# Kernel optimization log

Hardware: AMD Instinct MI355X
Metric: run time of the kernel (lower is better)

## Reference

```python
import jax, jax.numpy as jnp
import numpy as np

BN_EPS = 1e-5
ELU_ALPHA = 512.0  # bug-faithful: nn.ELU(in_channels) sets alpha=in_channels


def conv3x3(x, w):
    # NCHW input, OIHW kernel, stride 1, padding 1 (SAME for k=3)
    return jax.lax.conv_general_dilated(
        x, w, window_strides=(1, 1), padding=((1, 1), (1, 1)),
        dimension_numbers=('NCHW', 'OIHW', 'NCHW'))


def conv1x1(x, w, b):
    # 1x1 conv as a channel contraction
    return jnp.einsum('oc,bchw->bohw', w[:, :, 0, 0], x) + b[None, :, None, None]


def batchnorm(x, g, b, m, v):
    scale = g / jnp.sqrt(v + BN_EPS)
    return (x - m[None, :, None, None]) * scale[None, :, None, None] + b[None, :, None, None]


def cc_module(x, wq, bq, wk, bk, wv, bv, gamma):
    B, C, H, W = x.shape
    q = conv1x1(x, wq, bq)   # [B, C/8, H, W]
    k = conv1x1(x, wk, bk)   # [B, C/8, H, W]
    v = conv1x1(x, wv, bv)   # [B, C,   H, W]
    # column (H-axis) attention scores with -inf on the self-diagonal
    eH = jnp.einsum('bchw,bcgw->bhwg', q, k)              # [B,H,W,H]
    diag = jnp.eye(H, dtype=bool)[None, :, None, :]       # mask h == g
    eH = jnp.where(diag, -jnp.inf, eH)
    # row (W-axis) attention scores
    eW = jnp.einsum('bchw,bchv->bhwv', q, k)              # [B,H,W,W]
    att = jax.nn.softmax(jnp.concatenate([eH, eW], axis=-1), axis=-1)  # [B,H,W,H+W]
    aH, aW = att[..., :H], att[..., H:]
    oH = jnp.einsum('bcgw,bhwg->bchw', v, aH)
    oW = jnp.einsum('bchv,bhwv->bchw', v, aW)
    return gamma[0] * (oH + oW) + x


def setup_inputs() -> dict:
    key = jax.random.key(0)
    ks = jax.random.split(key, 20)
    B, Cin, H, W = 8, 512, 64, 64
    Ci = Cin // 4            # 128
    Cq = Ci // 8             # 16
    n = lambda k, s, sc: jax.random.normal(k, s, dtype=jnp.float32) * sc
    inp = {
        'x': n(ks[0], (B, Cin, H, W), 1.0),
        'conva_w': n(ks[1], (Ci, Cin, 3, 3), 0.02),
        'bn1_g': jax.random.uniform(ks[2], (Ci,)) + 0.5,
        'bn1_b': n(ks[3], (Ci,), 0.1),
        'bn1_m': n(ks[4], (Ci,), 0.1),
        'bn1_v': jax.random.uniform(ks[5], (Ci,)) + 0.5,
        'wq': n(ks[6], (Cq, Ci, 1, 1), 0.05),
        'bq': n(ks[7], (Cq,), 0.02),
        'wk': n(ks[8], (Cq, Ci, 1, 1), 0.05),
        'bk': n(ks[9], (Cq,), 0.02),
        'wv': n(ks[10], (Ci, Ci, 1, 1), 0.05),
        'bv': n(ks[11], (Ci,), 0.02),
        'cc_gamma': jnp.full((1,), 0.5, dtype=jnp.float32),
        'convb_w': n(ks[12], (Ci, Ci, 3, 3), 0.05),
        'bn2_g': jax.random.uniform(ks[13], (Ci,)) + 0.5,
        'bn2_b': n(ks[14], (Ci,), 0.1),
        'bn2_m': n(ks[15], (Ci,), 0.1),
        'bn2_v': jax.random.uniform(ks[16], (Ci,)) + 0.5,
        'bott_w': n(ks[17], (Cin, Cin + Ci, 3, 3), 0.02),
        'recurrence': 2,
    }
    return inp


def reference(x, conva_w, bn1_g, bn1_b, bn1_m, bn1_v,
              wq, bq, wk, bk, wv, bv, cc_gamma,
              convb_w, bn2_g, bn2_b, bn2_m, bn2_v,
              bott_w, recurrence):
    out = batchnorm(conv3x3(x, conva_w), bn1_g, bn1_b, bn1_m, bn1_v)
    for _ in range(int(recurrence)):
        out = cc_module(out, wq, bq, wk, bk, wv, bv, cc_gamma)
    out = batchnorm(conv3x3(out, convb_w), bn2_g, bn2_b, bn2_m, bn2_v)
    out = conv3x3(jnp.concatenate([x, out], axis=1), bott_w)
    # ELU with alpha = in_channels (faithful to nn.ELU(in_channels))
    return jnp.where(out > 0, out, ELU_ALPHA * jnp.expm1(out))
```

## Files before the change

### kernel.cpp

```cpp
#include <hip/hip_runtime.h>
#include <math.h>


typedef __attribute__((ext_vector_type(8)))  short short8;
typedef __attribute__((ext_vector_type(4)))  float f32x4;
typedef __attribute__((ext_vector_type(16))) float f32x16;

__device__ __forceinline__ unsigned short f2bf(float x) {
    unsigned u = __float_as_uint(x);
    unsigned r = u + 0x7FFFu + ((u >> 16) & 1u);
    return (unsigned short)(r >> 16);
}
__device__ __forceinline__ float bf2f(unsigned short h) {
    return __uint_as_float(((unsigned)h) << 16);
}
__device__ __forceinline__ void split2(float a, float b, unsigned& hi, unsigned& lo) {
    unsigned h;
    asm("v_cvt_pk_bf16_f32 %0, %1, %2" : "=v"(h) : "v"(a), "v"(b));
    float ra = a - __uint_as_float(h << 16);
    float rb = b - __uint_as_float(h & 0xffff0000u);
    unsigned l;
    asm("v_cvt_pk_bf16_f32 %0, %1, %2" : "=v"(l) : "v"(ra), "v"(rb));
    hi = h; lo = l;
}
__device__ __forceinline__ void gll16(const unsigned short* g, unsigned short* l) {
    __builtin_amdgcn_global_load_lds(
        (const __attribute__((address_space(1))) unsigned int*)g,
        (__attribute__((address_space(3))) unsigned int*)l, 16, 0, 0);
}

__global__ __launch_bounds__(256) void prep_bn_kernel(
        const float* g1, const float* b1, const float* m1, const float* v1,
        const float* g2, const float* b2, const float* m2, const float* v2,
        float* s1o, float* h1o, float* s2o, float* h2o) {
    int t = threadIdx.x;
    if (t < 128) {
        float s = g1[t] * __frsqrt_rn(v1[t] + 1e-5f);
        s1o[t] = s; h1o[t] = b1[t] - m1[t] * s;
    } else {
        int c = t - 128;
        float s = g2[c] * __frsqrt_rn(v2[c] + 1e-5f);
        s2o[c] = s; h2o[c] = b2[c] - m2[c] * s;
    }
}

__global__ __launch_bounds__(256) void prep_w2(
        const float* __restrict__ w, unsigned short* __restrict__ Wp, int CIN, int COUT) {
    int idx = blockIdx.x * 256 + threadIdx.x;
    if (idx >= COUT * CIN) return;
    int cout = idx / CIN, ci = idx - cout * CIN;
    int ck = ci >> 5, cl = ci & 31;
    #pragma unroll
    for (int tap = 0; tap < 9; ++tap) {
        float v = w[(size_t)idx * 9 + tap];
        unsigned short h = f2bf(v);
        unsigned short l = f2bf(v - bf2f(h));
        size_t rb = (((size_t)ck * 9 + tap) * 2 * COUT + cout) * 32;
        Wp[rb + cl] = h;
        Wp[rb + (size_t)COUT * 32 + cl] = l;
    }
}

__global__ __launch_bounds__(256) void prep_qkv_kernel(
        const float* __restrict__ wq, const float* __restrict__ wk,
        const float* __restrict__ wv,
        float* __restrict__ wqk_t, float* __restrict__ wv_t) {
    int e = blockIdx.x * 256 + threadIdx.x;
    if (e < 4096) {
        int ci = e >> 5, co = e & 31;
        wqk_t[e] = (co < 16) ? wq[co * 128 + ci] : wk[(co - 16) * 128 + ci];
    } else if (e < 4096 + 16384) {
        int e2 = e - 4096;
        int ci = e2 >> 7, co = e2 & 127;
        wv_t[e2] = wv[co * 128 + ci];
    }
}

__global__ __launch_bounds__(256) void transpose_split_kernel(
        const float* __restrict__ in, unsigned short* __restrict__ out, int NCH) {
    __shared__ float T[32][260];
    const int t = threadIdx.x;
    const int h0 = blockIdx.x * 4, b = blockIdx.y, ck = blockIdx.z;
    const float* base = in + (size_t)(b * NCH + ck) * 32 * 4096;
    const int ci = t >> 3, w0 = (t & 7) * 8;
    #pragma unroll
    for (int hh = 0; hh < 4; ++hh) {
        float4 u0 = *(const float4*)&base[(size_t)ci * 4096 + (h0 + hh) * 64 + w0];
        float4 u1 = *(const float4*)&base[(size_t)ci * 4096 + (h0 + hh) * 64 + w0 + 4];
        T[ci][hh * 65 + w0 + 0] = u0.x; T[ci][hh * 65 + w0 + 1] = u0.y;
        T[ci][hh * 65 + w0 + 2] = u0.z; T[ci][hh * 65 + w0 + 3] = u0.w;
        T[ci][hh * 65 + w0 + 4] = u1.x; T[ci][hh * 65 + w0 + 5] = u1.y;
        T[ci][hh * 65 + w0 + 6] = u1.z; T[ci][hh * 65 + w0 + 7] = u1.w;
    }
    __syncthreads();
    const int w = t & 63, hh2 = t >> 6;
    const int h = h0 + hh2;
    const size_t PL = (size_t)64 * 68 * 40;
    unsigned short* po = out + ((size_t)(b * NCH + ck) * 2) * PL;
    unsigned hi[16], lo[16];
    #pragma unroll
    for (int p = 0; p < 16; ++p) {
        float a = T[2 * p][hh2 * 65 + w];
        float c = T[2 * p + 1][hh2 * 65 + w];
        split2(a, c, hi[p], lo[p]);
    }
    uint4 zz = {0u, 0u, 0u, 0u};
    #pragma unroll
    for (int half = 0; half < 2; ++half) {
        bool ok = half ? (w >= 31) : (w <= 32);
        int slot = half ? (w - 31) : (w + 1);
        if (ok) {
            unsigned short* ph = po + ((size_t)h * 68 + half * 34 + slot) * 40;
            unsigned short* pl = ph + PL;
            #pragma unroll
            for (int q = 0; q < 4; ++q) {
                uint4 hv = {hi[q * 4], hi[q * 4 + 1], hi[q * 4 + 2], hi[q * 4 + 3]};
                uint4 lv = {lo[q * 4], lo[q * 4 + 1], lo[q * 4 + 2], lo[q * 4 + 3]};
                *(uint4*)(ph + q * 8) = hv;
                *(uint4*)(pl + q * 8) = lv;
            }
            *(uint4*)(ph + 32) = zz;
            *(uint4*)(pl + 32) = zz;
        }
    }
    if (w == 0 || w == 63) {
        int half = (w == 63);
        int slot = half ? 33 : 0;
        unsigned short* ph = po + ((size_t)h * 68 + half * 34 + slot) * 40;
        #pragma unroll
        for (int q = 0; q < 5; ++q) {
            *(uint4*)(ph + q * 8) = zz;
            *(uint4*)(ph + PL + q * 8) = zz;
        }
    }
}

template<int NCHUNK, int COUT, int EPI, int C1CH>
__global__ __launch_bounds__(128, 2) void conv3x3_g(
        const unsigned short* __restrict__ xt1, const unsigned short* __restrict__ xt2,
        const unsigned short* __restrict__ Wp,
        const float* __restrict__ bns, const float* __restrict__ bnb,
        float* __restrict__ out) {
    __shared__ __align__(16) unsigned short XS[2][6][34][40];
    const int t = threadIdx.x;
    const int lane = t & 63, ch = t >> 6;
    const int lw = lane & 31, kg = lane >> 5;
    const int h0 = blockIdx.x * 4;
    const int b  = blockIdx.y;
    const int cz = blockIdx.z >> 1, wz = blockIdx.z & 1;
    const int cb0 = cz * 128;
    const size_t XPLANE = (size_t)64 * 68 * 40;
    constexpr int HLSTR = 6 * 34 * 40;

    const f32x16 fz = {0.f,0.f,0.f,0.f,0.f,0.f,0.f,0.f,0.f,0.f,0.f,0.f,0.f,0.f,0.f,0.f};
    f32x16 acc[2][4];
    #pragma unroll
    for (int mt = 0; mt < 2; ++mt)
        #pragma unroll
        for (int r = 0; r < 4; ++r) acc[mt][r] = fz;

    #pragma unroll 1
    for (int chunk = 0; chunk < NCHUNK; ++chunk) {
        const unsigned short* xb = (chunk < C1CH)
            ? xt1 + ((size_t)(b * C1CH + chunk) * 2) * XPLANE
            : xt2 + ((size_t)(b * (NCHUNK - C1CH) + (chunk - C1CH)) * 2) * XPLANE;
        #pragma unroll
        for (int j = 0; j < 6; ++j) {
            const int grow = h0 - 1 + j;
            unsigned short* ld = &XS[ch][j][0][0];
            if (grow >= 0 && grow < 64) {
                const unsigned short* g = xb + (size_t)ch * XPLANE + ((size_t)grow * 68 + wz * 34) * 40;
                gll16(g + (size_t)lane * 8, ld + (size_t)lane * 8);
                gll16(g + (size_t)(64 + lane) * 8, ld + (size_t)(64 + lane) * 8);
                if (lane < 42)
                    gll16(g + (size_t)(128 + lane) * 8, ld + (size_t)(128 + lane) * 8);
            } else {
                short8 z = {};
                *(short8*)(ld + (size_t)lane * 8) = z;
                *(short8*)(ld + (size_t)(64 + lane) * 8) = z;
                if (lane < 42) *(short8*)(ld + (size_t)(128 + lane) * 8) = z;
            }
        }
        __syncthreads();

        const unsigned short* wbase = Wp + (size_t)chunk * (9 * 2 * (size_t)COUT * 32);
        const int crow = cb0 + ch * 64 + lw;
        short8 wc[8], wn[8];
        {
            const unsigned short* ph = wbase + ((size_t)0 * COUT + crow) * 32 + kg * 8;
            const unsigned short* pl = ph + (size_t)COUT * 32;
            wc[0] = *(const short8*)(ph);             wc[1] = *(const short8*)(ph + 32 * 32);
            wc[2] = *(const short8*)(pl);             wc[3] = *(const short8*)(pl + 32 * 32);
            wc[4] = *(const short8*)(ph + 16);        wc[5] = *(const short8*)(ph + 32 * 32 + 16);
            wc[6] = *(const short8*)(pl + 16);        wc[7] = *(const short8*)(pl + 32 * 32 + 16);
        }
        #pragma unroll 1
        for (int tap = 0; tap < 9; ++tap) {
            {
                const int tn = (tap < 8) ? tap + 1 : 0;
                const unsigned short* ph = wbase + ((size_t)(tn * 2) * COUT + crow) * 32 + kg * 8;
                const unsigned short* pl = ph + (size_t)COUT * 32;
                wn[0] = *(const short8*)(ph);         wn[1] = *(const short8*)(ph + 32 * 32);
                wn[2] = *(const short8*)(pl);         wn[3] = *(const short8*)(pl + 32 * 32);
                wn[4] = *(const short8*)(ph + 16);    wn[5] = *(const short8*)(ph + 32 * 32 + 16);
                wn[6] = *(const short8*)(pl + 16);    wn[7] = *(const short8*)(pl + 32 * 32 + 16);
            }
            const int kh = (tap < 3) ? 0 : ((tap < 6) ? 1 : 2);
            const int kw = tap - kh * 3;
            #pragma unroll
            for (int ks = 0; ks < 2; ++ks) {
                const short8 ah0 = wc[ks * 4 + 0], ah1 = wc[ks * 4 + 1];
                const short8 al0 = wc[ks * 4 + 2], al1 = wc[ks * 4 + 3];
                const int ko = ks * 16 + kg * 8;
                #pragma unroll
                for (int r = 0; r < 4; ++r) {
                    const unsigned short* xp = &XS[0][r + kh][lw + kw][ko];
                    short8 bh = *(const short8*)xp;
                    short8 bl = *(const short8*)(xp + HLSTR);
                    acc[0][r] = __builtin_amdgcn_mfma_f32_32x32x16_bf16(ah0, bh, acc[0][r], 0, 0, 0);
                    acc[1][r] = __builtin_amdgcn_mfma_f32_32x32x16_bf16(ah1, bh, acc[1][r], 0, 0, 0);
                    acc[0][r] = __builtin_amdgcn_mfma_f32_32x32x16_bf16(ah0, bl, acc[0][r], 0, 0, 0);
                    acc[1][r] = __builtin_amdgcn_mfma_f32_32x32x16_bf16(ah1, bl, acc[1][r], 0, 0, 0);
                    acc[0][r] = __builtin_amdgcn_mfma_f32_32x32x16_bf16(al0, bh, acc[0][r], 0, 0, 0);
                    acc[1][r] = __builtin_amdgcn_mfma_f32_32x32x16_bf16(al1, bh, acc[1][r], 0, 0, 0);
                }
            }
            #pragma unroll
            for (int i = 0; i < 8; ++i) wc[i] = wn[i];
        }
        __syncthreads();
    }
    #pragma unroll
    for (int mt = 0; mt < 2; ++mt) {
        #pragma unroll
        for (int r = 0; r < 4; ++r) {
            const int orow = h0 + r;
            #pragma unroll
            for (int reg = 0; reg < 16; ++reg) {
                const int m = (reg & 3) + 8 * (reg >> 2) + 4 * kg;
                const int cout = cb0 + ch * 64 + mt * 32 + m;
                float val = acc[mt][r][reg];
                if (EPI == 0) val = val * bns[cout] + bnb[cout];
                else          val = (val > 0.f) ? val : 512.0f * expm1f(val);
                out[((size_t)(b * COUT + cout) * 64 + orow) * 64 + wz * 32 + lw] = val;
            }
        }
    }
}

__global__ __launch_bounds__(256) void qk_kernel(
        const float* __restrict__ X, const float* __restrict__ wqk_t,
        const float* __restrict__ bq, const float* __restrict__ bk,
        float* __restrict__ q, float* __restrict__ k) {
    __shared__ float xls[128][64];
    __shared__ float wls[128][32];
    const int t = threadIdx.x;
    const int h = blockIdx.x, b = blockIdx.y;
    const float* xb = X + (size_t)b * 128 * 4096 + (size_t)h * 64;
    #pragma unroll
    for (int i = 0; i < 32; ++i) {
        int e = t + i * 256;
        xls[e >> 6][e & 63] = xb[(size_t)(e >> 6) * 4096 + (e & 63)];
    }
    #pragma unroll
    for (int i = 0; i < 16; ++i) {
        int e = t + i * 256;
        wls[e >> 5][e & 31] = wqk_t[e];
    }
    __syncthreads();
    const int w = t & 63, g = t >> 6;
    const int co0 = g * 8;
    float acc[8];
    #pragma unroll
    for (int c = 0; c < 8; ++c) acc[c] = 0.f;
    #pragma unroll 8
    for (int ci = 0; ci < 128; ++ci) {
        float xv = xls[ci][w];
        float4 wa = *(const float4*)&wls[ci][co0];
        float4 wb = *(const float4*)&wls[ci][co0 + 4];
        const float* pa = (const float*)&wa;
        const float* pb = (const float*)&wb;
        #pragma unroll
        for (int c = 0; c < 4; ++c) { acc[c] += pa[c] * xv; acc[4 + c] += pb[c] * xv; }
    }
    #pragma unroll
    for (int c = 0; c < 8; ++c) {
        int co = co0 + c;
        if (co < 16) q[((size_t)(b * 16 + co) * 64 + h) * 64 + w]      = acc[c] + bq[co];
        else         k[((size_t)(b * 16 + co - 16) * 64 + h) * 64 + w] = acc[c] + bk[co - 16];
    }
}

__global__ __launch_bounds__(256) void v_kernel(
        const float* __restrict__ X, const float* __restrict__ wv_t,
        const float* __restrict__ bv, float* __restrict__ v) {
    __shared__ float xls[16][64];
    __shared__ float wls[16][128];
    const int t = threadIdx.x;
    const int n0 = blockIdx.x * 64, b = blockIdx.y;
    const int wt = t & 15, ct = t >> 4;
    const float* xb = X + (size_t)b * 128 * 4096;
    float acc[8][4] = {};
    for (int ci0 = 0; ci0 < 128; ci0 += 16) {
        #pragma unroll
        for (int i = 0; i < 4; ++i) {
            int e = t + i * 256;
            xls[e >> 6][e & 63] = xb[(size_t)(ci0 + (e >> 6)) * 4096 + n0 + (e & 63)];
        }
        #pragma unroll
        for (int i = 0; i < 8; ++i) {
            int e = t + i * 256;
            wls[e >> 7][e & 127] = wv_t[(size_t)(ci0 + (e >> 7)) * 128 + (e & 127)];
        }
        __syncthreads();
        #pragma unroll 4
        for (int ci = 0; ci < 16; ++ci) {
            float4 xv = *(const float4*)&xls[ci][wt * 4];
            float4 wa = *(const float4*)&wls[ci][ct * 8];
            float4 wb = *(const float4*)&wls[ci][ct * 8 + 4];
            const float* px = (const float*)&xv;
            const float* pa = (const float*)&wa;
            const float* pb = (const float*)&wb;
            #pragma unroll
            for (int j = 0; j < 4; ++j)
                #pragma unroll
                for (int c = 0; c < 4; ++c) {
                    acc[c][j]     += pa[c] * px[j];
                    acc[4 + c][j] += pb[c] * px[j];
                }
        }
        __syncthreads();
    }
    #pragma unroll
    for (int c = 0; c < 8; ++c) {
        int co = ct * 8 + c;
        float bb = bv[co];
        float4 r = {acc[c][0] + bb, acc[c][1] + bb, acc[c][2] + bb, acc[c][3] + bb};
        *(float4*)&v[(size_t)(b * 128 + co) * 4096 + n0 + wt * 4] = r;
    }
}

__global__ __launch_bounds__(256) void eh_kernel(
        const float* __restrict__ q, const float* __restrict__ k,
        float* __restrict__ att) {
    __shared__ float qs[16][64];
    __shared__ float ks[16][64];
    const int t = threadIdx.x;
    const int w = blockIdx.x, b = blockIdx.y;
    #pragma unroll
    for (int i = 0; i < 4; ++i) {
        int e = t + i * 256;
        int c = e >> 6, h = e & 63;
        size_t idx = ((size_t)(b * 16 + c) * 64 + h) * 64 + w;
        qs[c][h] = q[idx];
        ks[c][h] = k[idx];
    }
    __syncthreads();
    const int g0 = (t & 15) * 4, h0 = (t >> 4) * 4;
    float acc[4][4] = {};
    #pragma unroll
    for (int c = 0; c < 16; ++c) {
        float4 qv = *(const float4*)&qs[c][h0];
        float4 kv = *(const float4*)&ks[c][g0];
        const float* pq = (const float*)&qv;
        const float* pk = (const float*)&kv;
        #pragma unroll
        for (int i = 0; i < 4; ++i)
            #pragma unroll
            for (int j = 0; j < 4; ++j) acc[i][j] += pq[i] * pk[j];
    }
    #pragma unroll
    for (int i = 0; i < 4; ++i) {
        int h = h0 + i;
        int dj = h - g0;
        if (dj >= 0 && dj < 4) acc[i][dj] = -1e30f;
        float4 r = {acc[i][0], acc[i][1], acc[i][2], acc[i][3]};
        *(float4*)&att[((size_t)(b * 64 + h) * 64 + w) * 128 + g0] = r;
    }
}

__global__ __launch_bounds__(256) void ew_softmax_kernel(
        const float* __restrict__ q, const float* __restrict__ k,
        float* __restrict__ att) {
    __shared__ float qs[16][64];
    __shared__ float ks[16][64];
    __shared__ float ehs[64][65];
    __shared__ float ews[64][65];
    __shared__ float sinv[64];
    const int t = threadIdx.x;
    const int h = blockIdx.x, b = blockIdx.y;
    const float* qb2 = q + (size_t)b * 65536 + (size_t)h * 64;
    const float* kb2 = k + (size_t)b * 65536 + (size_t)h * 64;
    #pragma unroll
    for (int i = 0; i < 4; ++i) {
        int e = t + i * 256;
        int c = e >> 6, wl = e & 63;
        qs[c][wl] = qb2[(size_t)c * 4096 + wl];
        ks[c][wl] = kb2[(size_t)c * 4096 + wl];
    }
    float* abase = att + (size_t)(b * 64 + h) * 64 * 128;
    #pragma unroll
    for (int i = 0; i < 16; ++i) {
        int e = t + i * 256;
        ehs[e >> 6][e & 63] = abase[(size_t)(e >> 6) * 128 + (e & 63)];
    }
    __syncthreads();
    const int tt0 = (t & 15) * 4, w0 = (t >> 4) * 4;
    float acc[4][4] = {};
    #pragma unroll
    for (int c = 0; c < 16; ++c) {
        float4 qv = *(const float4*)&qs[c][w0];
        float4 kv = *(const float4*)&ks[c][tt0];
        const float* pq = (const float*)&qv;
        const float* pk = (const float*)&kv;
        #pragma unroll
        for (int i = 0; i < 4; ++i)
            #pragma unroll
            for (int j = 0; j < 4; ++j) acc[i][j] += pq[i] * pk[j];
    }
    #pragma unroll
    for (int i = 0; i < 4; ++i)
        #pragma unroll
        for (int j = 0; j < 4; ++j) ews[w0 + i][tt0 + j] = acc[i][j];
    __syncthreads();
    const int r = t >> 2, qd = t & 3;
    float* src = (qd < 2) ? &ehs[r][qd * 32] : &ews[r][(qd - 2) * 32];
    float m = -3.0e38f;
    #pragma unroll
    for (int kk = 0; kk < 32; ++kk) m = fmaxf(m, src[kk]);
    m = fmaxf(m, __shfl_xor(m, 1));
    m = fmaxf(m, __shfl_xor(m, 2));
    float s = 0.f;
    #pragma unroll
    for (int kk = 0; kk < 32; ++kk) {
        float e = expf(src[kk] - m);
        src[kk] = e;
        s += e;
    }
    s += __shfl_xor(s, 1);
    s += __shfl_xor(s, 2);
    if (qd == 0) sinv[r] = 1.0f / s;
    __syncthreads();
    #pragma unroll
    for (int i = 0; i < 32; ++i) {
        int e = t + i * 256;
        int row = e >> 7, col = e & 127;
        float vsm = (col < 64) ? ehs[row][col] : ews[row][col - 64];
        abase[(size_t)row * 128 + col] = vsm * sinv[row];
    }
}

__global__ __launch_bounds__(256) void oh_kernel(
        const float* __restrict__ v, const float* __restrict__ att,
        float* __restrict__ ohb) {
    __shared__ float vs2[64][128];
    __shared__ float ah2[64][65];
    const int t = threadIdx.x;
    const int w = blockIdx.x, b = blockIdx.y;
    const float* vbp = v + (size_t)b * 524288 + w;
    #pragma unroll
    for (int i = 0; i < 32; ++i) {
        int e = t + i * 256;
        vs2[e >> 7][e & 127] = vbp[((size_t)(e & 127) * 64 + (e >> 7)) * 64];
    }
    const float* abp = att + ((size_t)b * 4096 + w) * 128;
    #pragma unroll
    for (int i = 0; i < 16; ++i) {
        int e = t + i * 256;
        ah2[e >> 6][e & 63] = abp[(size_t)(e >> 6) * 8192 + (e & 63)];
    }
    __syncthreads();
    const int h0 = (t & 15) * 4, c0 = (t >> 4) * 8;
    float acc[8][4] = {};
    for (int g = 0; g < 64; ++g) {
        float4 va  = *(const float4*)&vs2[g][c0];
        float4 vb4 = *(const float4*)&vs2[g][c0 + 4];
        const float* pa = (const float*)&va;
        const float* pb = (const float*)&vb4;
        float aj[4];
        #pragma unroll
        for (int j = 0; j < 4; ++j) aj[j] = ah2[h0 + j][g];
        #pragma unroll
        for (int j = 0; j < 4; ++j)
            #pragma unroll
            for (int i2 = 0; i2 < 4; ++i2) {
                acc[i2][j]     += pa[i2] * aj[j];
                acc[4 + i2][j] += pb[i2] * aj[j];
            }
    }
    #pragma unroll
    for (int i2 = 0; i2 < 8; ++i2)
        #pragma unroll
        for (int j = 0; j < 4; ++j)
            ohb[((size_t)(b * 128 + c0 + i2) * 64 + (h0 + j)) * 64 + w] = acc[i2][j];
}

__global__ __launch_bounds__(256) void ow_final_kernel(
        const float* __restrict__ v, const float* __restrict__ att,
        const float* __restrict__ ohb, const float* __restrict__ gamma,
        const float* __restrict__ Xin, float* __restrict__ Xout) {
    __shared__ float vs2[64][129];
    __shared__ float aws[64][65];
    const int t = threadIdx.x;
    const int h = blockIdx.x, b = blockIdx.y;
    const float* vbp = v + (size_t)b * 524288 + (size_t)h * 64;
    #pragma unroll
    for (int i = 0; i < 32; ++i) {
        int e = t + i * 256;
        vs2[e & 63][e >> 6] = vbp[(size_t)(e >> 6) * 4096 + (e & 63)];
    }
    const float* abp = att + ((size_t)(b * 64 + h) * 64) * 128 + 64;
    #pragma unroll
    for (int i = 0; i < 16; ++i) {
        int e = t + i * 256;
        aws[e >> 6][e & 63] = abp[(size_t)(e >> 6) * 128 + (e & 63)];
    }
    __syncthreads();
    const int w0 = (t & 15) * 4, c0 = (t >> 4) * 8;
    float acc[8][4] = {};
    for (int tt = 0; tt < 64; ++tt) {
        float vv[8];
        #pragma unroll
        for (int i2 = 0; i2 < 8; ++i2) vv[i2] = vs2[tt][c0 + i2];
        float aw[4];
        #pragma unroll
        for (int j = 0; j < 4; ++j) aw[j] = aws[w0 + j][tt];
        #pragma unroll
        for (int i2 = 0; i2 < 8; ++i2)
            #pragma unroll
            for (int j = 0; j < 4; ++j) acc[i2][j] += vv[i2] * aw[j];
    }
    const float gm = gamma[0];
    #pragma unroll
    for (int i2 = 0; i2 < 8; ++i2) {
        size_t base = ((size_t)(b * 128 + c0 + i2) * 64 + h) * 64 + w0;
        float4 oh4 = *(const float4*)&ohb[base];
        float4 xr  = *(const float4*)&Xin[base];
        const float* po = (const float*)&oh4;
        const float* px = (const float*)&xr;
        float4 r;
        float* pr = (float*)&r;
        #pragma unroll
        for (int j = 0; j < 4; ++j) pr[j] = gm * (acc[i2][j] + po[j]) + px[j];
        *(float4*)&Xout[base] = r;
    }
}

extern "C" void kernel_launch(void* const* d_in, const int* in_sizes, int n_in,
                              void* d_out, int out_size, void* d_ws, size_t ws_size,
                              hipStream_t stream) {
    const float* x       = (const float*)d_in[0];
    const float* conva_w = (const float*)d_in[1];
    const float* bn1_g   = (const float*)d_in[2];
    const float* bn1_b   = (const float*)d_in[3];
    const float* bn1_m   = (const float*)d_in[4];
    const float* bn1_v   = (const float*)d_in[5];
    const float* wq      = (const float*)d_in[6];
    const float* bq      = (const float*)d_in[7];
    const float* wk      = (const float*)d_in[8];
    const float* bk      = (const float*)d_in[9];
    const float* wv      = (const float*)d_in[10];
    const float* bv      = (const float*)d_in[11];
    const float* gamma   = (const float*)d_in[12];
    const float* convb_w = (const float*)d_in[13];
    const float* bn2_g   = (const float*)d_in[14];
    const float* bn2_b   = (const float*)d_in[15];
    const float* bn2_m   = (const float*)d_in[16];
    const float* bn2_v   = (const float*)d_in[17];
    const float* bott_w  = (const float*)d_in[18];

    float* ws   = (float*)d_ws;
    float* A    = ws;
    float* Bb   = A    + 4194304;
    float* vbuf = Bb   + 4194304;
    float* attb = vbuf + 4194304;
    float* ohb  = attb + 4194304;
    float* qb   = ohb  + 4194304;
    float* kb   = qb   + 524288;
    unsigned short* XT_x = (unsigned short*)(kb + 524288);
    float* after_xt = kb + 524288 + 22282240;
    unsigned short* Wp_a = (unsigned short*)after_xt;
    unsigned short* Wp_b = Wp_a + 1179648;
    unsigned short* Wp_c = Wp_b + 294912;
    float* wqk_t = (float*)(Wp_c + 5898240);
    float* wv_t  = wqk_t + 4096;
    float* bnsA  = wv_t + 16384;
    float* bnbA  = bnsA + 128;
    float* bnsB  = bnbA + 128;
    float* bnbB  = bnsB + 128;
    unsigned short* XT_cc = (unsigned short*)vbuf;
    unsigned short* XT_b  = XT_cc + 11141120;

    prep_bn_kernel<<<1, 256, 0, stream>>>(bn1_g, bn1_b, bn1_m, bn1_v,
                                          bn2_g, bn2_b, bn2_m, bn2_v,
                                          bnsA, bnbA, bnsB, bnbB);
    prep_w2<<<256, 256, 0, stream>>>(conva_w, Wp_a, 512, 128);
    prep_w2<<<64, 256, 0, stream>>>(convb_w, Wp_b, 128, 128);
    prep_w2<<<1280, 256, 0, stream>>>(bott_w, Wp_c, 640, 512);
    prep_qkv_kernel<<<80, 256, 0, stream>>>(wq, wk, wv, wqk_t, wv_t);

    transpose_split_kernel<<<dim3(16, 8, 16), 256, 0, stream>>>(x, XT_x, 16);

    conv3x3_g<16, 128, 0, 16><<<dim3(16, 8, 2), 128, 0, stream>>>(
        XT_x, nullptr, Wp_a, bnsA, bnbA, A);

    float* Xi = A;
    float* Xo = Bb;
    for (int it = 0; it < 2; ++it) {
        qk_kernel<<<dim3(64, 8), 256, 0, stream>>>(Xi, wqk_t, bq, bk, qb, kb);
        v_kernel<<<dim3(64, 8), 256, 0, stream>>>(Xi, wv_t, bv, vbuf);
        eh_kernel<<<dim3(64, 8), 256, 0, stream>>>(qb, kb, attb);
        ew_softmax_kernel<<<dim3(64, 8), 256, 0, stream>>>(qb, kb, attb);
        oh_kernel<<<dim3(64, 8), 256, 0, stream>>>(vbuf, attb, ohb);
        ow_final_kernel<<<dim3(64, 8), 256, 0, stream>>>(vbuf, attb, ohb, gamma, Xi, Xo);
        float* tmp = Xi; Xi = Xo; Xo = tmp;
    }

    transpose_split_kernel<<<dim3(16, 8, 4), 256, 0, stream>>>(Xi, XT_cc, 4);
    conv3x3_g<4, 128, 0, 4><<<dim3(16, 8, 2), 128, 0, stream>>>(
        XT_cc, nullptr, Wp_b, bnsB, bnbB, Bb);

    transpose_split_kernel<<<dim3(16, 8, 4), 256, 0, stream>>>(Bb, XT_b, 4);
    conv3x3_g<20, 512, 1, 16><<<dim3(16, 8, 8), 128, 0, stream>>>(
        XT_x, XT_b, Wp_c, nullptr, nullptr, (float*)d_out);
}
```

Measured before the change: 1.227 ms.

## Halve conv3x3 row tile, raise occupancy, make weight prefetch optional per launch

Each conv3x3 block now computes 2 output rows instead of 4, which halves the accumulator registers and shared-memory tile and doubles the grid. Launch bounds are raised to target 3–4 blocks per CU. A PF template flag lets the bottleneck conv skip the register double-buffered weight prefetch and load weights directly per k-step, saving registers. The MFMA issue order is regrouped so independent accumulators interleave. The trade-off is that each block reuses its weights and halo rows less, so more input rows are reloaded overall.

```diff
diff --git a/kernel.cpp b/kernel.cpp
--- a/kernel.cpp
+++ b/kernel.cpp
@@ -135,29 +135,29 @@
     }
 }
 
-template<int NCHUNK, int COUT, int EPI, int C1CH>
-__global__ __launch_bounds__(128, 2) void conv3x3_g(
+template<int NCHUNK, int COUT, int EPI, int C1CH, int PF>
+__global__ __launch_bounds__(128, PF ? 3 : 4) void conv3x3_g(
         const unsigned short* __restrict__ xt1, const unsigned short* __restrict__ xt2,
         const unsigned short* __restrict__ Wp,
         const float* __restrict__ bns, const float* __restrict__ bnb,
         float* __restrict__ out) {
-    __shared__ __align__(16) unsigned short XS[2][6][34][40];
+    __shared__ __align__(16) unsigned short XS[2][4][34][40];
     const int t = threadIdx.x;
     const int lane = t & 63, ch = t >> 6;
     const int lw = lane & 31, kg = lane >> 5;
-    const int h0 = blockIdx.x * 4;
+    const int h0 = blockIdx.x * 2;
     const int b  = blockIdx.y;
     const int cz = blockIdx.z >> 1, wz = blockIdx.z & 1;
     const int cb0 = cz * 128;
     const size_t XPLANE = (size_t)64 * 68 * 40;
-    constexpr int HLSTR = 6 * 34 * 40;
+    constexpr int HLSTR = 4 * 34 * 40;
 
     const f32x16 fz = {0.f,0.f,0.f,0.f,0.f,0.f,0.f,0.f,0.f,0.f,0.f,0.f,0.f,0.f,0.f,0.f};
-    f32x16 acc[2][4];
+    f32x16 acc[2][2];
     #pragma unroll
     for (int mt = 0; mt < 2; ++mt)
         #pragma unroll
-        for (int r = 0; r < 4; ++r) acc[mt][r] = fz;
+        for (int r = 0; r < 2; ++r) acc[mt][r] = fz;
 
     #pragma unroll 1
     for (int chunk = 0; chunk < NCHUNK; ++chunk) {
@@ -165,7 +165,7 @@
             ? xt1 + ((size_t)(b * C1CH + chunk) * 2) * XPLANE
             : xt2 + ((size_t)(b * (NCHUNK - C1CH) + (chunk - C1CH)) * 2) * XPLANE;
         #pragma unroll
-        for (int j = 0; j < 6; ++j) {
+        for (int j = 0; j < 4; ++j) {
             const int grow = h0 - 1 + j;
             unsigned short* ld = &XS[ch][j][0][0];
             if (grow >= 0 && grow < 64) {
@@ -186,54 +186,73 @@
         const unsigned short* wbase = Wp + (size_t)chunk * (9 * 2 * (size_t)COUT * 32);
         const int crow = cb0 + ch * 64 + lw;
         short8 wc[8], wn[8];
-        {
-            const unsigned short* ph = wbase + ((size_t)0 * COUT + crow) * 32 + kg * 8;
+        if (PF) {
+            const unsigned short* ph = wbase + (size_t)crow * 32 + kg * 8;
             const unsigned short* pl = ph + (size_t)COUT * 32;
-            wc[0] = *(const short8*)(ph);             wc[1] = *(const short8*)(ph + 32 * 32);
-            wc[2] = *(const short8*)(pl);             wc[3] = *(const short8*)(pl + 32 * 32);
-            wc[4] = *(const short8*)(ph + 16);        wc[5] = *(const short8*)(ph + 32 * 32 + 16);
-            wc[6] = *(const short8*)(pl + 16);        wc[7] = *(const short8*)(pl + 32 * 32 + 16);
+            wc[0] = *(const short8*)(ph);          wc[1] = *(const short8*)(ph + 32 * 32);
+            wc[2] = *(const short8*)(pl);          wc[3] = *(const short8*)(pl + 32 * 32);
+            wc[4] = *(const short8*)(ph + 16);     wc[5] = *(const short8*)(ph + 32 * 32 + 16);
+            wc[6] = *(const short8*)(pl + 16);     wc[7] = *(const short8*)(pl + 32 * 32 + 16);
         }
         #pragma unroll 1
         for (int tap = 0; tap < 9; ++tap) {
-            {
+            const unsigned short* ph = wbase + ((size_t)(tap * 2) * COUT + crow) * 32 + kg * 8;
+            const unsigned short* pl = ph + (size_t)COUT * 32;
+            if (PF) {
                 const int tn = (tap < 8) ? tap + 1 : 0;
-                const unsigned short* ph = wbase + ((size_t)(tn * 2) * COUT + crow) * 32 + kg * 8;
-                const unsigned short* pl = ph + (size_t)COUT * 32;
-                wn[0] = *(const short8*)(ph);         wn[1] = *(const short8*)(ph + 32 * 32);
-                wn[2] = *(const short8*)(pl);         wn[3] = *(const short8*)(pl + 32 * 32);
-                wn[4] = *(const short8*)(ph + 16);    wn[5] = *(const short8*)(ph + 32 * 32 + 16);
-                wn[6] = *(const short8*)(pl + 16);    wn[7] = *(const short8*)(pl + 32 * 32 + 16);
+                const unsigned short* phn = wbase + ((size_t)(tn * 2) * COUT + crow) * 32 + kg * 8;
+                const unsigned short* pln = phn + (size_t)COUT * 32;
+                wn[0] = *(const short8*)(phn);       wn[1] = *(const short8*)(phn + 32 * 32);
+                wn[2] = *(const short8*)(pln);       wn[3] = *(const short8*)(pln + 32 * 32);
+                wn[4] = *(const short8*)(phn + 16);  wn[5] = *(const short8*)(phn + 32 * 32 + 16);
+                wn[6] = *(const short8*)(pln + 16);  wn[7] = *(const short8*)(pln + 32 * 32 + 16);
             }
             const int kh = (tap < 3) ? 0 : ((tap < 6) ? 1 : 2);
             const int kw = tap - kh * 3;
             #pragma unroll
             for (int ks = 0; ks < 2; ++ks) {
-                const short8 ah0 = wc[ks * 4 + 0], ah1 = wc[ks * 4 + 1];
-                const short8 al0 = wc[ks * 4 + 2], al1 = wc[ks * 4 + 3];
+                short8 A0, A1, A2, A3;
+                if (PF) {
+                    A0 = wc[ks * 4 + 0]; A1 = wc[ks * 4 + 1];
+                    A2 = wc[ks * 4 + 2]; A3 = wc[ks * 4 + 3];
+                } else {
+                    A0 = *(const short8*)(ph + ks * 16);
+                    A1 = *(const short8*)(ph + 32 * 32 + ks * 16);
+                    A2 = *(const short8*)(pl + ks * 16);
+                    A3 = *(const short8*)(pl + 32 * 32 + ks * 16);
+                }
                 const int ko = ks * 16 + kg * 8;
+                short8 bh[2], bl[2];
                 #pragma unroll
-                for (int r = 0; r < 4; ++r) {
+                for (int r = 0; r < 2; ++r) {
                     const unsigned short* xp = &XS[0][r + kh][lw + kw][ko];
-                    short8 bh = *(const short8*)xp;
-                    short8 bl = *(const short8*)(xp + HLSTR);
-                    acc[0][r] = __builtin_amdgcn_mfma_f32_32x32x16_bf16(ah0, bh, acc[0][r], 0, 0, 0);
-                    acc[1][r] = __builtin_amdgcn_mfma_f32_32x32x16_bf16(ah1, bh, acc[1][r], 0, 0, 0);
-                    acc[0][r] = __builtin_amdgcn_mfma_f32_32x32x16_bf16(ah0, bl, acc[0][r], 0, 0, 0);
-                    acc[1][r] = __builtin_amdgcn_mfma_f32_32x32x16_bf16(ah1, bl, acc[1][r], 0, 0, 0);
-                    acc[0][r] = __builtin_amdgcn_mfma_f32_32x32x16_bf16(al0, bh, acc[0][r], 0, 0, 0);
-                    acc[1][r] = __builtin_amdgcn_mfma_f32_32x32x16_bf16(al1, bh, acc[1][r], 0, 0, 0);
+                    bh[r] = *(const short8*)xp;
+                    bl[r] = *(const short8*)(xp + HLSTR);
                 }
+                acc[0][0] = __builtin_amdgcn_mfma_f32_32x32x16_bf16(A0, bh[0], acc[0][0], 0, 0, 0);
+                acc[0][1] = __builtin_amdgcn_mfma_f32_32x32x16_bf16(A0, bh[1], acc[0][1], 0, 0, 0);
+                acc[1][0] = __builtin_amdgcn_mfma_f32_32x32x16_bf16(A1, bh[0], acc[1][0], 0, 0, 0);
+                acc[1][1] = __builtin_amdgcn_mfma_f32_32x32x16_bf16(A1, bh[1], acc[1][1], 0, 0, 0);
+                acc[0][0] = __builtin_amdgcn_mfma_f32_32x32x16_bf16(A0, bl[0], acc[0][0], 0, 0, 0);
+                acc[0][1] = __builtin_amdgcn_mfma_f32_32x32x16_bf16(A0, bl[1], acc[0][1], 0, 0, 0);
+                acc[1][0] = __builtin_amdgcn_mfma_f32_32x32x16_bf16(A1, bl[0], acc[1][0], 0, 0, 0);
+                acc[1][1] = __builtin_amdgcn_mfma_f32_32x32x16_bf16(A1, bl[1], acc[1][1], 0, 0, 0);
+                acc[0][0] = __builtin_amdgcn_mfma_f32_32x32x16_bf16(A2, bh[0], acc[0][0], 0, 0, 0);
+                acc[0][1] = __builtin_amdgcn_mfma_f32_32x32x16_bf16(A2, bh[1], acc[0][1], 0, 0, 0);
+                acc[1][0] = __builtin_amdgcn_mfma_f32_32x32x16_bf16(A3, bh[0], acc[1][0], 0, 0, 0);
+                acc[1][1] = __builtin_amdgcn_mfma_f32_32x32x16_bf16(A3, bh[1], acc[1][1], 0, 0, 0);
             }
-            #pragma unroll
-            for (int i = 0; i < 8; ++i) wc[i] = wn[i];
+            if (PF) {
+                #pragma unroll
+                for (int i = 0; i < 8; ++i) wc[i] = wn[i];
+            }
         }
         __syncthreads();
     }
     #pragma unroll
     for (int mt = 0; mt < 2; ++mt) {
         #pragma unroll
-        for (int r = 0; r < 4; ++r) {
+        for (int r = 0; r < 2; ++r) {
             const int orow = h0 + r;
             #pragma unroll
             for (int reg = 0; reg < 16; ++reg) {
@@ -601,7 +620,7 @@
 
     transpose_split_kernel<<<dim3(16, 8, 16), 256, 0, stream>>>(x, XT_x, 16);
 
-    conv3x3_g<16, 128, 0, 16><<<dim3(16, 8, 2), 128, 0, stream>>>(
+    conv3x3_g<16, 128, 0, 16, 1><<<dim3(32, 8, 2), 128, 0, stream>>>(
         XT_x, nullptr, Wp_a, bnsA, bnbA, A);
 
     float* Xi = A;
@@ -617,10 +636,10 @@
     }
 
     transpose_split_kernel<<<dim3(16, 8, 4), 256, 0, stream>>>(Xi, XT_cc, 4);
-    conv3x3_g<4, 128, 0, 4><<<dim3(16, 8, 2), 128, 0, stream>>>(
+    conv3x3_g<4, 128, 0, 4, 1><<<dim3(32, 8, 2), 128, 0, stream>>>(
         XT_cc, nullptr, Wp_b, bnsB, bnbB, Bb);
 
     transpose_split_kernel<<<dim3(16, 8, 4), 256, 0, stream>>>(Bb, XT_b, 4);
-    conv3x3_g<20, 512, 1, 16><<<dim3(16, 8, 8), 128, 0, stream>>>(
+    conv3x3_g<20, 512, 1, 16, 0><<<dim3(32, 8, 8), 128, 0, stream>>>(
         XT_x, XT_b, Wp_c, nullptr, nullptr, (float*)d_out);
 }
```

New measurement: 1.464 ms. 1.19x slower.
